# Performance work log

Measured on AMD Instinct MI355X. Metric: run time of the kernel, lower is better.

## Reference

```python
import jax, jax.numpy as jnp
import numpy as np

B, T, D_IN = 32, 1000, 1024
H = 32          # hidden_size
G = 4 * H       # gate dim (i,f,g,o)
L = 4           # num_layers


def setup_inputs() -> dict:
    key = jax.random.key(0)
    ks = jax.random.split(key, 12)
    s = 1.0 / np.sqrt(H)  # PyTorch LSTM init scale
    inp = {
        'x': jax.random.normal(ks[0], (B, T, D_IN), dtype=jnp.float32),
        # layer 0 (input dim 1024), [dir, ...]
        'w_ih0': jax.random.uniform(ks[1], (2, G, D_IN), minval=-s, maxval=s),
        'w_hh0': jax.random.uniform(ks[2], (2, G, H), minval=-s, maxval=s),
        'b_ih0': jax.random.uniform(ks[3], (2, G), minval=-s, maxval=s),
        'b_hh0': jax.random.uniform(ks[4], (2, G), minval=-s, maxval=s),
        # layers 1..3 (input dim 2H=64), [layer, dir, ...]
        'w_ih': jax.random.uniform(ks[5], (L - 1, 2, G, 2 * H), minval=-s, maxval=s),
        'w_hh': jax.random.uniform(ks[6], (L - 1, 2, G, H), minval=-s, maxval=s),
        'b_ih': jax.random.uniform(ks[7], (L - 1, 2, G), minval=-s, maxval=s),
        'b_hh': jax.random.uniform(ks[8], (L - 1, 2, G), minval=-s, maxval=s),
        # fc: Linear(64, 1)
        'fc_w': jax.random.uniform(ks[9], (1, 2 * H), minval=-0.125, maxval=0.125),
        'fc_b': jax.random.uniform(ks[10], (1,), minval=-0.125, maxval=0.125),
    }
    return inp


def _lstm_dir(x, wi, wh, b, reverse):
    # x: [B,T,Din]; wi: [4H,Din]; wh: [4H,H]; b: [4H]
    xp = jnp.einsum('btd,gd->tbg', x, wi) + b  # precomputed input proj [T,B,4H]
    whT = wh.T

    def step(carry, xt):
        h, c = carry
        g = xt + h @ whT
        i, f, gg, o = jnp.split(g, 4, axis=-1)  # PyTorch gate order i,f,g,o
        c = jax.nn.sigmoid(f) * c + jax.nn.sigmoid(i) * jnp.tanh(gg)
        h = jax.nn.sigmoid(o) * jnp.tanh(c)
        return (h, c), h

    init = (jnp.zeros((x.shape[0], H), x.dtype), jnp.zeros((x.shape[0], H), x.dtype))
    _, hs = jax.lax.scan(step, init, xp, reverse=reverse)  # hs aligned with input time order
    return hs.transpose(1, 0, 2)  # [B,T,H]


def _bilstm(x, wi, wh, bi, bh):
    fwd = _lstm_dir(x, wi[0], wh[0], bi[0] + bh[0], False)
    bwd = _lstm_dir(x, wi[1], wh[1], bi[1] + bh[1], True)
    return jnp.concatenate([fwd, bwd], axis=-1)  # [B,T,2H]


def reference(x, w_ih0, w_hh0, b_ih0, b_hh0, w_ih, w_hh, b_ih, b_hh, fc_w, fc_b):
    h = _bilstm(x, w_ih0, w_hh0, b_ih0, b_hh0)
    for l in range(L - 1):
        h = _bilstm(h, w_ih[l], w_hh[l], b_ih[l], b_hh[l])
    pooled = h.mean(axis=-2)           # [B,2H]
    return pooled @ fc_w.T + fc_b      # [B,1]
```

## Files before the change

kernel.cpp:

```cpp
#include <hip/hip_runtime.h>


#define TB 1000
#define LOG2E 1.44269504088896340736f

typedef int   v2i __attribute__((ext_vector_type(2)));
typedef float v2f __attribute__((ext_vector_type(2)));

__device__ __forceinline__ float fexp2(float x) {
#if __has_builtin(__builtin_amdgcn_exp2f)
    return __builtin_amdgcn_exp2f(x);
#else
    return exp2f(x);
#endif
}

__device__ __forceinline__ float lane_xor32(float v, bool pickx) {
    v2i r = __builtin_amdgcn_permlane32_swap(__float_as_int(v), __float_as_int(v),
                                             false, false);
    return __int_as_float(pickx ? r[0] : r[1]);
}

__global__ __launch_bounds__(256)
void gemm_proj(const float* __restrict__ A, int K,
               const float* __restrict__ W,
               const float* __restrict__ bi,
               const float* __restrict__ bh,
               float* __restrict__ xpT)
{
    __shared__ __align__(16) float As[32][68];
    __shared__ __align__(16) float Bs[32][132];

    const int tid = threadIdx.x;
    const int m0 = blockIdx.x * 64;
    const int n0 = blockIdx.y * 128;
    const int tx = tid & 15;
    const int ty = tid >> 4;

    float acc[8][4];
#pragma unroll
    for (int i = 0; i < 8; ++i)
#pragma unroll
        for (int jj = 0; jj < 4; ++jj) acc[i][jj] = 0.0f;

    const int ar = tid >> 3;
    const int ak = (tid & 7) * 4;
    const int wr = tid >> 1;
    const int wk = (tid & 1) * 16;

    for (int k0 = 0; k0 < K; k0 += 32) {
        float4 a0 = *(const float4*)(A + (size_t)(m0 + ar) * K + k0 + ak);
        float4 a1 = *(const float4*)(A + (size_t)(m0 + ar + 32) * K + k0 + ak);
        const float* wp = W + (size_t)(n0 + wr) * K + k0 + wk;
        float4 w0 = *(const float4*)(wp + 0);
        float4 w1 = *(const float4*)(wp + 4);
        float4 w2 = *(const float4*)(wp + 8);
        float4 w3 = *(const float4*)(wp + 12);

        __syncthreads();
        As[ak + 0][ar] = a0.x; As[ak + 1][ar] = a0.y;
        As[ak + 2][ar] = a0.z; As[ak + 3][ar] = a0.w;
        As[ak + 0][ar + 32] = a1.x; As[ak + 1][ar + 32] = a1.y;
        As[ak + 2][ar + 32] = a1.z; As[ak + 3][ar + 32] = a1.w;
        {
            float wv[16] = {w0.x, w0.y, w0.z, w0.w,
                            w1.x, w1.y, w1.z, w1.w,
                            w2.x, w2.y, w2.z, w2.w,
                            w3.x, w3.y, w3.z, w3.w};
#pragma unroll
            for (int q = 0; q < 16; ++q) Bs[wk + q][wr] = wv[q];
        }
        __syncthreads();

#pragma unroll
        for (int kk = 0; kk < 32; ++kk) {
            float4 av = *(const float4*)&As[kk][tx * 4];
            float4 b0 = *(const float4*)&Bs[kk][ty * 8];
            float4 b1 = *(const float4*)&Bs[kk][ty * 8 + 4];
            float bn[8] = {b0.x, b0.y, b0.z, b0.w, b1.x, b1.y, b1.z, b1.w};
#pragma unroll
            for (int ni = 0; ni < 8; ++ni) {
                acc[ni][0] = fmaf(av.x, bn[ni], acc[ni][0]);
                acc[ni][1] = fmaf(av.y, bn[ni], acc[ni][1]);
                acc[ni][2] = fmaf(av.z, bn[ni], acc[ni][2]);
                acc[ni][3] = fmaf(av.w, bn[ni], acc[ni][3]);
            }
        }
    }

    const int dir = n0 >> 7;
    const int mbase = m0 + tx * 4;
    const int bidx = mbase / 1000;
    const int ttq = mbase - bidx * 1000;
#pragma unroll
    for (int ni = 0; ni < 8; ++ni) {
        const int n = n0 + ty * 8 + ni;
        const float bias = bi[n] + bh[n];
        const float sc = (((n >> 5) & 3) == 2) ? (-2.0f * LOG2E) : (-LOG2E);
        float* row = xpT + ((size_t)((dir * 32 + bidx) * 128) + (n & 127)) * TB;
        if (dir == 0) {
            float4 o = {(acc[ni][0] + bias) * sc, (acc[ni][1] + bias) * sc,
                        (acc[ni][2] + bias) * sc, (acc[ni][3] + bias) * sc};
            *(float4*)(row + ttq) = o;
        } else {
            float4 o = {(acc[ni][3] + bias) * sc, (acc[ni][2] + bias) * sc,
                        (acc[ni][1] + bias) * sc, (acc[ni][0] + bias) * sc};
            *(float4*)(row + (TB - 4 - ttq)) = o;
        }
    }
}

template<int MODE>
__global__ __launch_bounds__(64)
void lstm_rec(const float* __restrict__ xpT,
              const float* __restrict__ whh,
              float* __restrict__ hout,
              float* __restrict__ hsum)
{
    __shared__ __align__(16) float hsh[32];

    const int blk  = blockIdx.x;
    const int dir  = blk >> 5;
    const int b    = blk & 31;
    const int lane = threadIdx.x & 63;
    const int j    = lane & 31;
    const int up   = lane >> 5;
    const int r0   = j + up * 64;
    const int r1   = r0 + 32;

    v2i det = __builtin_amdgcn_permlane32_swap(lane, lane, false, false);
    const bool pickx = (det[0] == (lane ^ 32));

    const float sA = up ? (-2.0f * LOG2E) : (-LOG2E);
    const float sB = -LOG2E;
    v2f wa[16], wb[16];
    {
        const float* wp0 = whh + (size_t)(dir * 128 + r0) * 32;
        const float* wp1 = whh + (size_t)(dir * 128 + r1) * 32;
#pragma unroll
        for (int q = 0; q < 8; ++q) {
            float4 v = *(const float4*)(wp0 + q * 4);
            wa[2 * q + 0][0] = v.x * sA; wa[2 * q + 0][1] = v.y * sA;
            wa[2 * q + 1][0] = v.z * sA; wa[2 * q + 1][1] = v.w * sA;
            float4 u = *(const float4*)(wp1 + q * 4);
            wb[2 * q + 0][0] = u.x * sB; wb[2 * q + 0][1] = u.y * sB;
            wb[2 * q + 1][0] = u.z * sB; wb[2 * q + 1][1] = u.w * sB;
        }
    }

    const float* pa = xpT + ((size_t)blk * 128 + r0) * TB;
    const float* pb = xpT + ((size_t)blk * 128 + r1) * TB;

    float4 A0 = *(const float4*)(pa + 0);
    float4 B0 = *(const float4*)(pb + 0);
    float4 A1 = *(const float4*)(pa + 4);
    float4 B1 = *(const float4*)(pb + 4);

    const float mA = up ?  2.0f : 1.0f;
    const float mB = up ? -1.0f : 0.0f;

    float cs = 0.0f, h = 0.0f, hacc = 0.0f;
    float* hq = hout + ((size_t)b * TB + (dir ? TB - 1 : 0)) * 64 + dir * 32 + j;
    const int hstep = dir ? -64 : 64;

    const unsigned lds_z  = (unsigned)(size_t)&hsh[0];
    const unsigned lds_wa = lds_z + 4u * (unsigned)j;

    float4 hv0, hv1, hv2, hv3, hv4v, hv5, hv6, hv7;

#define DS_WRITE_H() \
    asm volatile("ds_write_b32 %0, %1" :: "v"(lds_wa), "v"(h))

#define DS_ISSUE_READS() do {                                                   \
    asm volatile("ds_read_b128 %0, %1 offset:0"   : "=v"(hv0)  : "v"(lds_z));   \
    asm volatile("ds_read_b128 %0, %1 offset:16"  : "=v"(hv1)  : "v"(lds_z));   \
    asm volatile("ds_read_b128 %0, %1 offset:32"  : "=v"(hv2)  : "v"(lds_z));   \
    asm volatile("ds_read_b128 %0, %1 offset:48"  : "=v"(hv3)  : "v"(lds_z));   \
    asm volatile("ds_read_b128 %0, %1 offset:64"  : "=v"(hv4v) : "v"(lds_z));   \
    asm volatile("ds_read_b128 %0, %1 offset:80"  : "=v"(hv5)  : "v"(lds_z));   \
    asm volatile("ds_read_b128 %0, %1 offset:96"  : "=v"(hv6)  : "v"(lds_z));   \
    asm volatile("ds_read_b128 %0, %1 offset:112" : "=v"(hv7)  : "v"(lds_z));   \
    } while (0)

#define MVG(HV, CNT, I0, I1, Q)                                                 \
    asm volatile("s_waitcnt lgkmcnt(" #CNT ")");                                \
    __builtin_amdgcn_sched_barrier(0);                                          \
    {                                                                           \
        v2f h0_ = {HV.x, HV.y};                                                 \
        v2f h1_ = {HV.z, HV.w};                                                 \
        qa[I0] = __builtin_elementwise_fma(h0_, wa[2*Q],   qa[I0]);             \
        qb[I0] = __builtin_elementwise_fma(h0_, wb[2*Q],   qb[I0]);             \
        qa[I1] = __builtin_elementwise_fma(h1_, wa[2*Q+1], qa[I1]);             \
        qb[I1] = __builtin_elementwise_fma(h1_, wb[2*Q+1], qb[I1]);             \
    }

    DS_WRITE_H();
    DS_ISSUE_READS();

#define LSTM_STEP(GA, GB) do {                                                  \
        v2f qa[4], qb[4];                                                       \
        qa[0] = v2f{(GA), 0.0f}; qa[1] = v2f{0.f, 0.f};                         \
        qa[2] = v2f{0.f, 0.f};   qa[3] = v2f{0.f, 0.f};                         \
        qb[0] = v2f{(GB), 0.0f}; qb[1] = v2f{0.f, 0.f};                         \
        qb[2] = v2f{0.f, 0.f};   qb[3] = v2f{0.f, 0.f};                         \
        MVG(hv0,  7, 0, 1, 0)                                                   \
        MVG(hv1,  6, 2, 3, 1)                                                   \
        MVG(hv2,  5, 0, 1, 2)                                                   \
        MVG(hv3,  4, 2, 3, 3)                                                   \
        MVG(hv4v, 3, 0, 1, 4)                                                   \
        MVG(hv5,  2, 2, 3, 5)                                                   \
        MVG(hv6,  1, 0, 1, 6)                                                   \
        MVG(hv7,  0, 2, 3, 7)                                                   \
        v2f sa = (qa[0] + qa[2]) + (qa[1] + qa[3]);                             \
        v2f sb = (qb[0] + qb[2]) + (qb[1] + qb[3]);                             \
        float g0 = sa[0] + sa[1];                                               \
        float g1 = sb[0] + sb[1];                                               \
        float s0 = __builtin_amdgcn_rcpf(1.0f + fexp2(g0));                     \
        float v0 = fmaf(mA, s0, mB);               \
        float v1 = __builtin_amdgcn_rcpf(1.0f + fexp2(g1));  \
        float o0 = lane_xor32(v0, pickx);                                       \
        float o1 = lane_xor32(v1, pickx);                                       \
        float P  = v0 * o0;                        \
        float Ps = P * (-2.0f * LOG2E);                                         \
        float sf = up ? o1 : v1;                                                \
        float so = up ? v1 : o1;                                                \
        cs = fmaf(sf, cs, Ps);                            \
        float r_ = __builtin_amdgcn_rcpf(1.0f + fexp2(cs));                     \
        float so2 = so + so;                                                    \
        h = fmaf(so2, r_, -so);                             \
        DS_WRITE_H();                                                           \
        DS_ISSUE_READS();                                                       \
        if (MODE == 0) {                                                        \
            asm volatile("global_store_dword %0, %1, off" :: "v"(hq), "v"(h));  \
        } else {                                                                \
            hacc += h;                                                          \
        }                                                                       \
        hq += hstep;                                                            \
    } while (0)

    for (int it = 0; it < 125; ++it) {
        const int base = it * 8;
        const int offn0 = min(base + 8,  TB - 4);
        const int offn1 = min(base + 12, TB - 4);
        float4 NA0 = *(const float4*)(pa + offn0);
        float4 NB0 = *(const float4*)(pb + offn0);
        float4 NA1 = *(const float4*)(pa + offn1);
        float4 NB1 = *(const float4*)(pb + offn1);

        LSTM_STEP(A0.x, B0.x);
        LSTM_STEP(A0.y, B0.y);
        LSTM_STEP(A0.z, B0.z);
        LSTM_STEP(A0.w, B0.w);
        LSTM_STEP(A1.x, B1.x);
        LSTM_STEP(A1.y, B1.y);
        LSTM_STEP(A1.z, B1.z);
        LSTM_STEP(A1.w, B1.w);

        A0 = NA0; B0 = NB0; A1 = NA1; B1 = NB1;
    }
#undef LSTM_STEP
#undef MVG
#undef DS_ISSUE_READS
#undef DS_WRITE_H

    asm volatile("s_waitcnt lgkmcnt(0)" ::: "memory");

    if (MODE == 1) hsum[b * 64 + dir * 32 + j] = hacc;
}

__global__ __launch_bounds__(64)
void final_fc(const float* __restrict__ hsum,
              const float* __restrict__ fcw,
              const float* __restrict__ fcb,
              float* __restrict__ out)
{
    int b = blockIdx.x;
    int l = threadIdx.x;
    float v = hsum[b * 64 + l] * (1.0f / (float)TB) * fcw[l];
#pragma unroll
    for (int off = 32; off > 0; off >>= 1)
        v += __shfl_down(v, off, 64);
    if (l == 0) out[b] = v + fcb[0];
}

extern "C" void kernel_launch(void* const* d_in, const int* in_sizes, int n_in,
                              void* d_out, int out_size, void* d_ws, size_t ws_size,
                              hipStream_t stream)
{
    const float* x    = (const float*)d_in[0];
    const float* wih0 = (const float*)d_in[1];
    const float* whh0 = (const float*)d_in[2];
    const float* bih0 = (const float*)d_in[3];
    const float* bhh0 = (const float*)d_in[4];
    const float* wih  = (const float*)d_in[5];
    const float* whh  = (const float*)d_in[6];
    const float* bih  = (const float*)d_in[7];
    const float* bhh  = (const float*)d_in[8];
    const float* fcw  = (const float*)d_in[9];
    const float* fcb  = (const float*)d_in[10];
    float* out = (float*)d_out;

    float* ws = (float*)d_ws;
    float* xp = ws;
    float* hb = ws + 8192000;
    float* hs = ws + 8192000 + 2048000;

    dim3 gb(500, 2);

    gemm_proj<<<gb, 256, 0, stream>>>(x, 1024, wih0, bih0, bhh0, xp);
    lstm_rec<0><<<64, 64, 0, stream>>>(xp, whh0, hb, hs);

    for (int l = 1; l < 4; ++l) {
        const float* wl  = wih + (size_t)(l - 1) * 2 * 128 * 64;
        const float* whl = whh + (size_t)(l - 1) * 2 * 128 * 32;
        const float* b1  = bih + (size_t)(l - 1) * 256;
        const float* b2  = bhh + (size_t)(l - 1) * 256;
        gemm_proj<<<gb, 256, 0, stream>>>(hb, 64, wl, b1, b2, xp);
        if (l == 3) lstm_rec<1><<<64, 64, 0, stream>>>(xp, whl, hb, hs);
        else        lstm_rec<0><<<64, 64, 0, stream>>>(xp, whl, hb, hs);
    }

    final_fc<<<32, 64, 0, stream>>>(hs, fcw, fcb, out);
}
```

Baseline: 1.030 ms.

## Double-buffer projection GEMM with direct global-to-LDS loads and XOR swizzle

Rewrites the input-projection GEMM main loop to load A and W tiles straight into LDS with global_load_lds, using two buffers so the next K-chunk is fetched while the current one is computed. Tiles are kept in row-major K-contiguous layout with an XOR swizzle to avoid LDS bank conflicts, replacing the register-staged transposed stores. This removes one of the two barriers per iteration and the register round-trip, at the cost of doubled LDS use and a different inner-loop access pattern. The recurrent LSTM part is untouched, so the gain is limited to the GEMM share of the total time.

Result: slower. 1.212 ms (+17.6%).

```diff
diff --git a/kernel.cpp b/kernel.cpp
--- a/kernel.cpp
+++ b/kernel.cpp
@@ -19,6 +19,13 @@
     v2i r = __builtin_amdgcn_permlane32_swap(__float_as_int(v), __float_as_int(v),
                                              false, false);
     return __int_as_float(pickx ? r[0] : r[1]);
+}
+
+__device__ __forceinline__ void gload_lds16(const float* g, float* lds_base) {
+    __builtin_amdgcn_global_load_lds(
+        (const __attribute__((address_space(1))) void*)g,
+        (__attribute__((address_space(3))) void*)lds_base,
+        16, 0, 0);
 }
 
 __global__ __launch_bounds__(256)
@@ -28,14 +35,15 @@
                const float* __restrict__ bh,
                float* __restrict__ xpT)
 {
-    __shared__ __align__(16) float As[32][68];
-    __shared__ __align__(16) float Bs[32][132];
+    __shared__ __align__(16) float As[2][64 * 32];
+    __shared__ __align__(16) float Ws[2][128 * 32];
 
     const int tid = threadIdx.x;
     const int m0 = blockIdx.x * 64;
     const int n0 = blockIdx.y * 128;
     const int tx = tid & 15;
     const int ty = tid >> 4;
+    const int wv = tid >> 6;
 
     float acc[8][4];
 #pragma unroll
@@ -43,50 +51,76 @@
 #pragma unroll
         for (int jj = 0; jj < 4; ++jj) acc[i][jj] = 0.0f;
 
-    const int ar = tid >> 3;
-    const int ak = (tid & 7) * 4;
-    const int wr = tid >> 1;
-    const int wk = (tid & 1) * 16;
-
-    for (int k0 = 0; k0 < K; k0 += 32) {
-        float4 a0 = *(const float4*)(A + (size_t)(m0 + ar) * K + k0 + ak);
-        float4 a1 = *(const float4*)(A + (size_t)(m0 + ar + 32) * K + k0 + ak);
-        const float* wp = W + (size_t)(n0 + wr) * K + k0 + wk;
-        float4 w0 = *(const float4*)(wp + 0);
-        float4 w1 = *(const float4*)(wp + 4);
-        float4 w2 = *(const float4*)(wp + 8);
-        float4 w3 = *(const float4*)(wp + 12);
-
-        __syncthreads();
-        As[ak + 0][ar] = a0.x; As[ak + 1][ar] = a0.y;
-        As[ak + 2][ar] = a0.z; As[ak + 3][ar] = a0.w;
-        As[ak + 0][ar + 32] = a1.x; As[ak + 1][ar + 32] = a1.y;
-        As[ak + 2][ar + 32] = a1.z; As[ak + 3][ar + 32] = a1.w;
-        {
-            float wv[16] = {w0.x, w0.y, w0.z, w0.w,
-                            w1.x, w1.y, w1.z, w1.w,
-                            w2.x, w2.y, w2.z, w2.w,
-                            w3.x, w3.y, w3.z, w3.w};
-#pragma unroll
-            for (int q = 0; q < 16; ++q) Bs[wk + q][wr] = wv[q];
-        }
-        __syncthreads();
-
-#pragma unroll
-        for (int kk = 0; kk < 32; ++kk) {
-            float4 av = *(const float4*)&As[kk][tx * 4];
-            float4 b0 = *(const float4*)&Bs[kk][ty * 8];
-            float4 b1 = *(const float4*)&Bs[kk][ty * 8 + 4];
-            float bn[8] = {b0.x, b0.y, b0.z, b0.w, b1.x, b1.y, b1.z, b1.w};
-#pragma unroll
-            for (int ni = 0; ni < 8; ++ni) {
-                acc[ni][0] = fmaf(av.x, bn[ni], acc[ni][0]);
-                acc[ni][1] = fmaf(av.y, bn[ni], acc[ni][1]);
-                acc[ni][2] = fmaf(av.z, bn[ni], acc[ni][2]);
-                acc[ni][3] = fmaf(av.w, bn[ni], acc[ni][3]);
-            }
-        }
-    }
+    const int slot = tid & 7;
+    const int rA   = tid >> 3;
+    const int kqA  = slot ^ ((rA >> 2) & 7);
+    const float* gA0 = A + (size_t)(m0 + rA) * K + kqA * 4;
+    const float* gA1 = gA0 + (size_t)32 * K;
+
+    const int swWe = wv;
+    const int swWo = (4 + wv) & 7;
+    const float* gW0 = W + (size_t)(n0 +  0 + rA) * K + (slot ^ swWe) * 4;
+    const float* gW1 = W + (size_t)(n0 + 32 + rA) * K + (slot ^ swWo) * 4;
+    const float* gW2 = W + (size_t)(n0 + 64 + rA) * K + (slot ^ swWe) * 4;
+    const float* gW3 = W + (size_t)(n0 + 96 + rA) * K + (slot ^ swWo) * 4;
+
+#define STAGE(BUF, KOFF) do {                                                   \
+        gload_lds16(gA0 + (KOFF), &As[BUF][(0 * 4 + wv) * 256]);                \
+        gload_lds16(gA1 + (KOFF), &As[BUF][(1 * 4 + wv) * 256]);                \
+        gload_lds16(gW0 + (KOFF), &Ws[BUF][(0 * 4 + wv) * 256]);                \
+        gload_lds16(gW1 + (KOFF), &Ws[BUF][(1 * 4 + wv) * 256]);                \
+        gload_lds16(gW2 + (KOFF), &Ws[BUF][(2 * 4 + wv) * 256]);                \
+        gload_lds16(gW3 + (KOFF), &Ws[BUF][(3 * 4 + wv) * 256]);                \
+    } while (0)
+
+    STAGE(0, 0);
+    asm volatile("s_waitcnt vmcnt(0)" ::: "memory");
+    __syncthreads();
+
+    const int sA4 = tx & 7;
+    const int sW4 = ty & 7;
+
+    const int nch = K >> 5;
+    int p = 0;
+    for (int ch = 0; ch < nch; ++ch) {
+        const bool more = (ch + 1 < nch);
+        if (more) {
+            if (p == 0) STAGE(1, (ch + 1) * 32);
+            else        STAGE(0, (ch + 1) * 32);
+        }
+
+        const float* Ap = As[p];
+        const float* Wp = Ws[p];
+#pragma unroll
+        for (int kq = 0; kq < 8; ++kq) {
+            float4 av[4];
+            float4 bv[8];
+            const int ka = (kq ^ sA4) * 4;
+            const int kw = (kq ^ sW4) * 4;
+#pragma unroll
+            for (int mi = 0; mi < 4; ++mi)
+                av[mi] = *(const float4*)(Ap + (tx * 4 + mi) * 32 + ka);
+#pragma unroll
+            for (int ni = 0; ni < 8; ++ni)
+                bv[ni] = *(const float4*)(Wp + (ty * 8 + ni) * 32 + kw);
+#pragma unroll
+            for (int ni = 0; ni < 8; ++ni)
+#pragma unroll
+                for (int mi = 0; mi < 4; ++mi) {
+                    acc[ni][mi] = fmaf(av[mi].x, bv[ni].x, acc[ni][mi]);
+                    acc[ni][mi] = fmaf(av[mi].y, bv[ni].y, acc[ni][mi]);
+                    acc[ni][mi] = fmaf(av[mi].z, bv[ni].z, acc[ni][mi]);
+                    acc[ni][mi] = fmaf(av[mi].w, bv[ni].w, acc[ni][mi]);
+                }
+        }
+
+        if (more) {
+            asm volatile("s_waitcnt vmcnt(0)" ::: "memory");
+            __syncthreads();
+        }
+        p ^= 1;
+    }
+#undef STAGE
 
     const int dir = n0 >> 7;
     const int mbase = m0 + tx * 4;
```
